# Optimization experiments

Measured on AMD Instinct MI355X. Metric: run time of the kernel, lower is better.

The kernel has to match this reference:

```python
import jax, jax.numpy as jnp
import numpy as np

BITS = 8
EPS = 1e-08
D_IN = 4096
D_OUT = 4096


def setup_inputs() -> dict:
    key = jax.random.key(0)
    k1, k2, k3 = jax.random.split(key, 3)
    hidden_states = jax.random.normal(k1, (4, 2048, D_IN), dtype=jnp.float32)
    # Pre-quantized (dequantized-value) weight buffer, as the module stores it in float
    qmax = 2 ** (BITS - 1) - 1
    w = jax.random.normal(k2, (D_IN, D_OUT), dtype=jnp.float32) * 0.02
    w_scale = jnp.max(jnp.abs(w)) / qmax
    weight_quantized = jnp.clip(jnp.round(w / w_scale), -qmax, qmax) * w_scale
    bias = jax.random.normal(k3, (D_OUT,), dtype=jnp.float32) * 0.01
    x_scale = jnp.asarray(3.0, dtype=jnp.float32)  # calibrated activation maxabs
    return {
        "hidden_states": hidden_states,
        "weight_quantized": weight_quantized,
        "x_scale": x_scale,
        "bias": bias,
    }


def _quantize_maxabs(x, scale, bits, eps):
    # scalar max-abs quantization with a fixed (calibrated) scale
    qmax = 2 ** (bits - 1) - 1
    step = jnp.maximum(scale, eps) / qmax
    return jnp.clip(jnp.round(x / step), -qmax, qmax) * step


def reference(hidden_states, weight_quantized, x_scale, bias):
    orig_shape = hidden_states.shape[:-1]
    d = hidden_states.shape[-1]
    x_flat = hidden_states.reshape(-1, d)
    x_q = _quantize_maxabs(x_flat, x_scale, BITS, EPS).astype(weight_quantized.dtype)
    out = x_q @ weight_quantized  # [tokens, d_out]
    out = out + bias.astype(out.dtype)[None, :]
    out = out.astype(hidden_states.dtype)
    return out.reshape(*orig_shape, weight_quantized.shape[1])
```

## Files before the change

kernel.cpp:

```cpp
#include <hip/hip_runtime.h>
#include <hip/hip_bf16.h>
#include <cstdint>

#define D_IN  4096
#define D_OUT 4096

typedef __attribute__((ext_vector_type(4)))  int   i32x4;

typedef const __attribute__((address_space(1))) unsigned g_u32;
typedef __attribute__((address_space(3))) unsigned       l_u32;

__global__ void prep_kernel(const float* __restrict__ W, int nw,
                            const float* __restrict__ x,
                            char* __restrict__ xq,
                            const float* __restrict__ xscale, int nx,
                            unsigned* __restrict__ wsp) {
    int tid = threadIdx.x;
    if (blockIdx.x < 1024) {
        __shared__ float red[256];
        float m = 0.f;
        for (int i = (blockIdx.x * 256 + tid) * 4; i < nw; i += 1024 * 256 * 4) {
            float4 v = *(const float4*)(W + i);
            m = fmaxf(m, fmaxf(fmaxf(fabsf(v.x), fabsf(v.y)),
                               fmaxf(fabsf(v.z), fabsf(v.w))));
        }
        red[tid] = m; __syncthreads();
        for (int s = 128; s > 0; s >>= 1) {
            if (tid < s) red[tid] = fmaxf(red[tid], red[tid + s]);
            __syncthreads();
        }
        if (tid == 0) atomicMax(wsp, __float_as_uint(red[0]));
    } else {
        int i = ((blockIdx.x - 1024) * 256 + tid) * 4;
        if (i >= nx) return;
        float inv = 127.0f / fmaxf(xscale[0], 1e-8f);
        float4 v = *(const float4*)(x + i);
        char4 o;
        o.x = (char)fminf(fmaxf(rintf(v.x * inv), -127.f), 127.f);
        o.y = (char)fminf(fmaxf(rintf(v.y * inv), -127.f), 127.f);
        o.z = (char)fminf(fmaxf(rintf(v.z * inv), -127.f), 127.f);
        o.w = (char)fminf(fmaxf(rintf(v.w * inv), -127.f), 127.f);
        *(char4*)(xq + i) = o;
    }
}

__global__ void convW_kernel(const float* __restrict__ W,
                             char* __restrict__ Wt,
                             const unsigned* __restrict__ wsp) {
    __shared__ float tile[64][65];
    const float wmax = __uint_as_float(wsp[0]);
    const float inv  = 127.0f / wmax;
    const int n0 = blockIdx.x * 64, k0 = blockIdx.y * 64;
    const int t = threadIdx.x;
    {
        const int r = t >> 2, c0 = (t & 3) * 16;
        const float* src = W + (size_t)(k0 + r) * D_OUT + n0 + c0;
#pragma unroll
        for (int j = 0; j < 4; ++j) {
            float4 v = *(const float4*)(src + j * 4);
            tile[r][c0 + j * 4 + 0] = v.x;
            tile[r][c0 + j * 4 + 1] = v.y;
            tile[r][c0 + j * 4 + 2] = v.z;
            tile[r][c0 + j * 4 + 3] = v.w;
        }
    }
    __syncthreads();
    {
        const int n = t >> 2, kc = (t & 3) * 16;
        int4 pk;
        int* pw = (int*)&pk;
#pragma unroll
        for (int w = 0; w < 4; ++w) {
            unsigned word = 0;
#pragma unroll
            for (int j = 0; j < 4; ++j) {
                int q = (int)rintf(tile[kc + w * 4 + j][n] * inv);
                word |= ((unsigned)(unsigned char)(char)q) << (8 * j);
            }
            pw[w] = (int)word;
        }
        *(int4*)(Wt + (size_t)(n0 + n) * D_IN + k0 + kc) = pk;
    }
}

__global__ __launch_bounds__(512, 2)
void gemm_kernel(const char* __restrict__ A,
                 const char* __restrict__ Bt,
                 const float* __restrict__ bias,
                 const float* __restrict__ xscale,
                 const unsigned* __restrict__ wsp,
                 float* __restrict__ C, int M) {
    constexpr int K = D_IN, N = D_OUT;
    constexpr int NT = K / 128;
    __shared__ char lds[2 * 65536];

    const int tid  = threadIdx.x;
    const int lane = tid & 63;
    const int wid  = tid >> 6;
    const int wr   = wid >> 2;
    const int wc   = wid & 3;

    const int nTn = N / 256;
    const int nwg = gridDim.x;
    int bid = blockIdx.x;
    int q8 = nwg >> 3, r8 = nwg & 7;
    int xcd = bid & 7, idx = bid >> 3;
    int swz = (xcd < r8 ? xcd * (q8 + 1) : r8 * (q8 + 1) + (xcd - r8) * q8) + idx;
    const int tm = swz / nTn, tn = swz % nTn;
    const int row0 = tm * 256, col0 = tn * 256;

    int srcOff[4], dstOff[4];
#pragma unroll
    for (int i = 0; i < 4; ++i) {
        int p  = (i * 512 + tid) * 16;
        int sw = p ^ (((p >> 7) & 7) << 4);
        dstOff[i] = p;
        srcOff[i] = (sw >> 7) * K + (sw & 127);
    }

    const char* srcA = A  + (size_t)row0 * K;
    const char* srcB = Bt + (size_t)col0 * K;
    char* ldsb = lds;

    auto STAGE4 = [&](const char* src, char* dst) {
#pragma unroll
        for (int i = 0; i < 4; ++i)
            __builtin_amdgcn_global_load_lds((g_u32*)(src + srcOff[i]),
                                             (l_u32*)(dst + dstOff[i]), 16, 0, 0);
    };
    auto STAGE2 = [&](const char* src, char* dst) {
#pragma unroll
        for (int i = 0; i < 2; ++i)
            __builtin_amdgcn_global_load_lds((g_u32*)(src + srcOff[i]),
                                             (l_u32*)(dst + dstOff[i]), 16, 0, 0);
    };

    STAGE2(srcB, ldsb + 32768);
    STAGE4(srcA, ldsb);
    STAGE2(srcB + 128 * K, ldsb + 32768 + 16384);
    STAGE2(srcB + 128,     ldsb + 65536 + 32768);
    STAGE4(srcA + 128,     ldsb + 65536);

    i32x4 acc[8][4];
#pragma unroll
    for (int m = 0; m < 8; ++m)
#pragma unroll
        for (int n = 0; n < 4; ++n) acc[m][n] = (i32x4){0, 0, 0, 0};

    const int cp0 = (((lane >> 4) << 4)) ^ ((lane & 7) << 4);
    const int cp1 = cp0 ^ 64;
    const int aBase = (wr * 128 + (lane & 15)) * 128;
    const int bBase = (wc * 64  + (lane & 15)) * 128;

    asm volatile("s_waitcnt vmcnt(6)" ::: "memory");

    auto KITER = [&](int t, char* cur, char* nxt) {
        i32x4 a[4][2], b01[2][2], b23[2][2];
        const char* cA = cur;
        const char* cB = cur + 32768;

        __builtin_amdgcn_s_barrier();
        if (t + 1 < NT) STAGE2(srcB + 128 * K + (t + 1) * 128, nxt + 32768 + 16384);

#pragma unroll
        for (int n = 0; n < 2; ++n) {
            b01[n][0] = *(const i32x4*)(cB + bBase + n * 2048 + cp0);
            b01[n][1] = *(const i32x4*)(cB + bBase + n * 2048 + cp1);
        }
#pragma unroll
        for (int m = 0; m < 4; ++m) {
            a[m][0] = *(const i32x4*)(cA + aBase + m * 2048 + cp0);
            a[m][1] = *(const i32x4*)(cA + aBase + m * 2048 + cp1);
        }
#pragma unroll
        for (int n = 0; n < 2; ++n) {
            b23[n][0] = *(const i32x4*)(cB + bBase + 4096 + n * 2048 + cp0);
            b23[n][1] = *(const i32x4*)(cB + bBase + 4096 + n * 2048 + cp1);
        }

        __builtin_amdgcn_s_setprio(1);
#pragma unroll
        for (int m = 0; m < 4; ++m)
#pragma unroll
            for (int n = 0; n < 2; ++n) {
                acc[m][n] = __builtin_amdgcn_mfma_i32_16x16x64_i8(a[m][0], b01[n][0], acc[m][n], 0, 0, 0);
                acc[m][n] = __builtin_amdgcn_mfma_i32_16x16x64_i8(a[m][1], b01[n][1], acc[m][n], 0, 0, 0);
            }
#pragma unroll
        for (int m = 0; m < 4; ++m)
#pragma unroll
            for (int n = 0; n < 2; ++n) {
                acc[m][n + 2] = __builtin_amdgcn_mfma_i32_16x16x64_i8(a[m][0], b23[n][0], acc[m][n + 2], 0, 0, 0);
                acc[m][n + 2] = __builtin_amdgcn_mfma_i32_16x16x64_i8(a[m][1], b23[n][1], acc[m][n + 2], 0, 0, 0);
            }
#pragma unroll
        for (int m = 0; m < 4; ++m) {
            a[m][0] = *(const i32x4*)(cA + aBase + 8192 + m * 2048 + cp0);
            a[m][1] = *(const i32x4*)(cA + aBase + 8192 + m * 2048 + cp1);
        }
#pragma unroll
        for (int m = 0; m < 4; ++m)
#pragma unroll
            for (int n = 0; n < 2; ++n) {
                acc[m + 4][n + 2] = __builtin_amdgcn_mfma_i32_16x16x64_i8(a[m][0], b23[n][0], acc[m + 4][n + 2], 0, 0, 0);
                acc[m + 4][n + 2] = __builtin_amdgcn_mfma_i32_16x16x64_i8(a[m][1], b23[n][1], acc[m + 4][n + 2], 0, 0, 0);
            }
#pragma unroll
        for (int m = 0; m < 4; ++m)
#pragma unroll
            for (int n = 0; n < 2; ++n) {
                acc[m + 4][n] = __builtin_amdgcn_mfma_i32_16x16x64_i8(a[m][0], b01[n][0], acc[m + 4][n], 0, 0, 0);
                acc[m + 4][n] = __builtin_amdgcn_mfma_i32_16x16x64_i8(a[m][1], b01[n][1], acc[m + 4][n], 0, 0, 0);
            }
        __builtin_amdgcn_s_setprio(0);

        __builtin_amdgcn_s_barrier();
        if (t + 2 < NT) {
            STAGE2(srcB + (t + 2) * 128, cur + 32768);
            STAGE4(srcA + (t + 2) * 128, cur);
            asm volatile("s_waitcnt vmcnt(6)" ::: "memory");
        } else {
            asm volatile("s_waitcnt vmcnt(0)" ::: "memory");
        }
    };

    for (int t = 0; t < NT; t += 2) {
        KITER(t,     ldsb,         ldsb + 65536);
        KITER(t + 1, ldsb + 65536, ldsb);
    }

    const float wmax  = __uint_as_float(wsp[0]);
    const float scale = (fmaxf(xscale[0], 1e-8f) * (1.0f / 127.0f)) * (wmax * (1.0f / 127.0f));
    const int lr = (lane >> 4) * 4, lc = lane & 15;
#pragma unroll
    for (int n = 0; n < 4; ++n) {
        int col = col0 + wc * 64 + n * 16 + lc;
        float bv = bias[col];
#pragma unroll
        for (int m = 0; m < 8; ++m) {
            int rowb = row0 + wr * 128 + m * 16 + lr;
            i32x4 v = acc[m][n];
#pragma unroll
            for (int r2 = 0; r2 < 4; ++r2)
                C[(size_t)(rowb + r2) * N + col] = (float)v[r2] * scale + bv;
        }
    }
}

extern "C" void kernel_launch(void* const* d_in, const int* in_sizes, int n_in,
                              void* d_out, int out_size, void* d_ws, size_t ws_size,
                              hipStream_t stream) {
    const float* x      = (const float*)d_in[0];
    const float* W      = (const float*)d_in[1];
    const float* xscale = (const float*)d_in[2];
    const float* bias   = (const float*)d_in[3];
    float* out = (float*)d_out;

    const int nx = in_sizes[0];
    const int nw = in_sizes[1];
    const int M  = nx / D_IN;

    char*     xq  = (char*)d_ws;
    char*     Wt  = (char*)d_ws + (size_t)nx;
    unsigned* wsp = (unsigned*)((char*)d_ws + (size_t)nx + nw);

    hipMemsetAsync(wsp, 0, 4, stream);

    int qblocks = nx / 4 / 256;
    prep_kernel<<<1024 + qblocks, 256, 0, stream>>>(W, nw, x, xq, xscale, nx, wsp);

    dim3 tb(256);
    dim3 tg(D_OUT / 64, D_IN / 64);
    convW_kernel<<<tg, tb, 0, stream>>>(W, Wt, wsp);

    int grid = (M / 256) * (D_OUT / 256);
    gemm_kernel<<<grid, 512, 0, stream>>>(xq, Wt, bias, xscale, wsp, out, M);
}
```

Before: 200.8 us.

## Split K-tile staging into half-tile loads interleaved with MFMA quadrants

Restructures the int8 GEMM main loop so that global-to-LDS staging for the next K tiles is issued in four half-tile chunks, each placed between the MFMA quadrants that no longer read that LDS region. The goal is to spread memory traffic evenly across compute and overlap it better with matrix work, instead of issuing most loads in one burst after all MFMAs. The cost is more barriers and lgkmcnt waits per tile, which may add synchronisation stalls.

```diff
diff --git a/kernel.cpp b/kernel.cpp
--- a/kernel.cpp
+++ b/kernel.cpp
@@ -109,9 +109,9 @@
     const int tm = swz / nTn, tn = swz % nTn;
     const int row0 = tm * 256, col0 = tn * 256;
 
-    int srcOff[4], dstOff[4];
-#pragma unroll
-    for (int i = 0; i < 4; ++i) {
+    int srcOff[2], dstOff[2];
+#pragma unroll
+    for (int i = 0; i < 2; ++i) {
         int p  = (i * 512 + tid) * 16;
         int sw = p ^ (((p >> 7) & 7) << 4);
         dstOff[i] = p;
@@ -120,26 +120,23 @@
 
     const char* srcA = A  + (size_t)row0 * K;
     const char* srcB = Bt + (size_t)col0 * K;
-    char* ldsb = lds;
-
-    auto STAGE4 = [&](const char* src, char* dst) {
-#pragma unroll
-        for (int i = 0; i < 4; ++i)
-            __builtin_amdgcn_global_load_lds((g_u32*)(src + srcOff[i]),
-                                             (l_u32*)(dst + dstOff[i]), 16, 0, 0);
-    };
-    auto STAGE2 = [&](const char* src, char* dst) {
+    char* buf0 = lds;
+    char* buf1 = lds + 65536;
+
+    auto STAGEH = [&](const char* src, char* dst) {
 #pragma unroll
         for (int i = 0; i < 2; ++i)
             __builtin_amdgcn_global_load_lds((g_u32*)(src + srcOff[i]),
                                              (l_u32*)(dst + dstOff[i]), 16, 0, 0);
     };
 
-    STAGE2(srcB, ldsb + 32768);
-    STAGE4(srcA, ldsb);
-    STAGE2(srcB + 128 * K, ldsb + 32768 + 16384);
-    STAGE2(srcB + 128,     ldsb + 65536 + 32768);
-    STAGE4(srcA + 128,     ldsb + 65536);
+    STAGEH(srcA,               buf0);
+    STAGEH(srcA + 128 * K,     buf0 + 16384);
+    STAGEH(srcB,               buf0 + 32768);
+    STAGEH(srcB + 128 * K,     buf0 + 49152);
+    STAGEH(srcB + 128,         buf1 + 32768);
+    STAGEH(srcB + 128 * K + 128, buf1 + 49152);
+    STAGEH(srcA + 128,         buf1);
 
     i32x4 acc[8][4];
 #pragma unroll
@@ -153,80 +150,94 @@
     const int bBase = (wc * 64  + (lane & 15)) * 128;
 
     asm volatile("s_waitcnt vmcnt(6)" ::: "memory");
-
-    auto KITER = [&](int t, char* cur, char* nxt) {
-        i32x4 a[4][2], b01[2][2], b23[2][2];
+    __builtin_amdgcn_s_barrier();
+
+    auto TILE = [&](int t, char* cur, char* nxt) {
+        i32x4 aR[4][2], b01[2][2], b23[2][2];
         const char* cA = cur;
         const char* cB = cur + 32768;
-
-        __builtin_amdgcn_s_barrier();
-        if (t + 1 < NT) STAGE2(srcB + 128 * K + (t + 1) * 128, nxt + 32768 + 16384);
-
+        const bool st2 = (t + 2 < NT);
+
+#pragma unroll
+        for (int m = 0; m < 4; ++m) {
+            aR[m][0] = *(const i32x4*)(cA + aBase + m * 2048 + cp0);
+            aR[m][1] = *(const i32x4*)(cA + aBase + m * 2048 + cp1);
+        }
 #pragma unroll
         for (int n = 0; n < 2; ++n) {
             b01[n][0] = *(const i32x4*)(cB + bBase + n * 2048 + cp0);
             b01[n][1] = *(const i32x4*)(cB + bBase + n * 2048 + cp1);
         }
 #pragma unroll
-        for (int m = 0; m < 4; ++m) {
-            a[m][0] = *(const i32x4*)(cA + aBase + m * 2048 + cp0);
-            a[m][1] = *(const i32x4*)(cA + aBase + m * 2048 + cp1);
-        }
-#pragma unroll
         for (int n = 0; n < 2; ++n) {
             b23[n][0] = *(const i32x4*)(cB + bBase + 4096 + n * 2048 + cp0);
             b23[n][1] = *(const i32x4*)(cB + bBase + 4096 + n * 2048 + cp1);
         }
-
-        __builtin_amdgcn_s_setprio(1);
-#pragma unroll
-        for (int m = 0; m < 4; ++m)
-#pragma unroll
-            for (int n = 0; n < 2; ++n) {
-                acc[m][n] = __builtin_amdgcn_mfma_i32_16x16x64_i8(a[m][0], b01[n][0], acc[m][n], 0, 0, 0);
-                acc[m][n] = __builtin_amdgcn_mfma_i32_16x16x64_i8(a[m][1], b01[n][1], acc[m][n], 0, 0, 0);
-            }
-#pragma unroll
-        for (int m = 0; m < 4; ++m)
-#pragma unroll
-            for (int n = 0; n < 2; ++n) {
-                acc[m][n + 2] = __builtin_amdgcn_mfma_i32_16x16x64_i8(a[m][0], b23[n][0], acc[m][n + 2], 0, 0, 0);
-                acc[m][n + 2] = __builtin_amdgcn_mfma_i32_16x16x64_i8(a[m][1], b23[n][1], acc[m][n + 2], 0, 0, 0);
-            }
+        if (t + 1 < NT) STAGEH(srcA + 128 * K + (t + 1) * 128, nxt + 16384);
+        __builtin_amdgcn_s_barrier();
+        __builtin_amdgcn_s_setprio(1);
+#pragma unroll
+        for (int m = 0; m < 4; ++m)
+#pragma unroll
+            for (int n = 0; n < 2; ++n) {
+                acc[m][n] = __builtin_amdgcn_mfma_i32_16x16x64_i8(aR[m][0], b01[n][0], acc[m][n], 0, 0, 0);
+                acc[m][n] = __builtin_amdgcn_mfma_i32_16x16x64_i8(aR[m][1], b01[n][1], acc[m][n], 0, 0, 0);
+            }
+        __builtin_amdgcn_s_setprio(0);
+        asm volatile("s_waitcnt lgkmcnt(0)" ::: "memory");
+        __builtin_amdgcn_s_barrier();
+
+        if (st2) STAGEH(srcB + (t + 2) * 128, cur + 32768);
+        __builtin_amdgcn_s_barrier();
+        __builtin_amdgcn_s_setprio(1);
+#pragma unroll
+        for (int m = 0; m < 4; ++m)
+#pragma unroll
+            for (int n = 0; n < 2; ++n) {
+                acc[m][n + 2] = __builtin_amdgcn_mfma_i32_16x16x64_i8(aR[m][0], b23[n][0], acc[m][n + 2], 0, 0, 0);
+                acc[m][n + 2] = __builtin_amdgcn_mfma_i32_16x16x64_i8(aR[m][1], b23[n][1], acc[m][n + 2], 0, 0, 0);
+            }
+        __builtin_amdgcn_s_setprio(0);
+        __builtin_amdgcn_s_barrier();
+
 #pragma unroll
         for (int m = 0; m < 4; ++m) {
-            a[m][0] = *(const i32x4*)(cA + aBase + 8192 + m * 2048 + cp0);
-            a[m][1] = *(const i32x4*)(cA + aBase + 8192 + m * 2048 + cp1);
-        }
-#pragma unroll
-        for (int m = 0; m < 4; ++m)
-#pragma unroll
-            for (int n = 0; n < 2; ++n) {
-                acc[m + 4][n + 2] = __builtin_amdgcn_mfma_i32_16x16x64_i8(a[m][0], b23[n][0], acc[m + 4][n + 2], 0, 0, 0);
-                acc[m + 4][n + 2] = __builtin_amdgcn_mfma_i32_16x16x64_i8(a[m][1], b23[n][1], acc[m + 4][n + 2], 0, 0, 0);
-            }
-#pragma unroll
-        for (int m = 0; m < 4; ++m)
-#pragma unroll
-            for (int n = 0; n < 2; ++n) {
-                acc[m + 4][n] = __builtin_amdgcn_mfma_i32_16x16x64_i8(a[m][0], b01[n][0], acc[m + 4][n], 0, 0, 0);
-                acc[m + 4][n] = __builtin_amdgcn_mfma_i32_16x16x64_i8(a[m][1], b01[n][1], acc[m + 4][n], 0, 0, 0);
-            }
-        __builtin_amdgcn_s_setprio(0);
-
-        __builtin_amdgcn_s_barrier();
-        if (t + 2 < NT) {
-            STAGE2(srcB + (t + 2) * 128, cur + 32768);
-            STAGE4(srcA + (t + 2) * 128, cur);
-            asm volatile("s_waitcnt vmcnt(6)" ::: "memory");
-        } else {
-            asm volatile("s_waitcnt vmcnt(0)" ::: "memory");
-        }
+            aR[m][0] = *(const i32x4*)(cA + aBase + 8192 + m * 2048 + cp0);
+            aR[m][1] = *(const i32x4*)(cA + aBase + 8192 + m * 2048 + cp1);
+        }
+        if (st2) STAGEH(srcB + 128 * K + (t + 2) * 128, cur + 49152);
+        __builtin_amdgcn_s_barrier();
+        __builtin_amdgcn_s_setprio(1);
+#pragma unroll
+        for (int m = 0; m < 4; ++m)
+#pragma unroll
+            for (int n = 0; n < 2; ++n) {
+                acc[m + 4][n + 2] = __builtin_amdgcn_mfma_i32_16x16x64_i8(aR[m][0], b23[n][0], acc[m + 4][n + 2], 0, 0, 0);
+                acc[m + 4][n + 2] = __builtin_amdgcn_mfma_i32_16x16x64_i8(aR[m][1], b23[n][1], acc[m + 4][n + 2], 0, 0, 0);
+            }
+        __builtin_amdgcn_s_setprio(0);
+        asm volatile("s_waitcnt lgkmcnt(0)" ::: "memory");
+        __builtin_amdgcn_s_barrier();
+
+        if (st2) STAGEH(srcA + (t + 2) * 128, cur);
+        __builtin_amdgcn_s_barrier();
+        __builtin_amdgcn_s_setprio(1);
+#pragma unroll
+        for (int m = 0; m < 4; ++m)
+#pragma unroll
+            for (int n = 0; n < 2; ++n) {
+                acc[m + 4][n] = __builtin_amdgcn_mfma_i32_16x16x64_i8(aR[m][0], b01[n][0], acc[m + 4][n], 0, 0, 0);
+                acc[m + 4][n] = __builtin_amdgcn_mfma_i32_16x16x64_i8(aR[m][1], b01[n][1], acc[m + 4][n], 0, 0, 0);
+            }
+        __builtin_amdgcn_s_setprio(0);
+        if (st2) { asm volatile("s_waitcnt vmcnt(6)" ::: "memory"); }
+        else     { asm volatile("s_waitcnt vmcnt(0)" ::: "memory"); }
+        __builtin_amdgcn_s_barrier();
     };
 
     for (int t = 0; t < NT; t += 2) {
-        KITER(t,     ldsb,         ldsb + 65536);
-        KITER(t + 1, ldsb + 65536, ldsb);
+        TILE(t,     buf0, buf1);
+        TILE(t + 1, buf1, buf0);
     }
 
     const float wmax  = __uint_as_float(wsp[0]);
```

Result: no change. 200.4 us (-0.2%).
